# Performance work log

Hardware: AMD Instinct MI355X
Metric: run time of the kernel (lower is better)

Reference implementation:

```python
import jax, jax.numpy as jnp
import numpy as np

L = 2        # layer_depth
H = 128      # rnn_size (== embedding dim)
V = 50257    # vocab_size
B = 100      # batch_size
T = 50       # seq_length


def setup_inputs() -> dict:
    key = jax.random.key(0)
    ks = jax.random.split(key, 8)
    inp = {
        'input_data': jax.random.randint(ks[0], (B, T), 0, V, dtype=jnp.int32),
        # embedding ~ U(-0.08, 0.08) as in the original
        'embedding': jax.random.uniform(ks[1], (V, H), jnp.float32, -0.08, 0.08),
        # per-layer GRU params; input dim == H for every layer
        'gate_k': jax.random.normal(ks[2], (L, 2 * H, 2 * H), jnp.float32) * 0.05,
        'gate_b': jnp.ones((L, 2 * H), jnp.float32),  # TF GRUCell gate bias init = 1.0
        'cand_k': jax.random.normal(ks[3], (L, 2 * H, H), jnp.float32) * 0.05,
        'cand_b': jnp.zeros((L, H), jnp.float32),
        'softmax_w': jax.random.normal(ks[4], (V, H), jnp.float32) * 0.05,
        'softmax_b': jnp.zeros((V,), jnp.float32),
    }
    return inp


def _gru_scan(x_bth, gate_k, gate_b, cand_k, cand_b):
    # x_bth: [B, T, H] embedded inputs. Stacked L-layer GRU, TF GRUCell math:
    #   r,u = sigmoid([x,h] @ Wg + bg);  c = tanh([x, r*h] @ Wc + bc)
    #   h' = u*h + (1-u)*c
    x_tbh = jnp.swapaxes(x_bth, 0, 1)  # [T, B, H]
    h0 = jnp.zeros((L, x_bth.shape[0], H), x_bth.dtype)

    def step(hs, x_t):
        inp = x_t
        new_hs = []
        for l in range(L):
            h = hs[l]
            g = jax.nn.sigmoid(jnp.concatenate([inp, h], -1) @ gate_k[l] + gate_b[l])
            r, u = g[:, :H], g[:, H:]
            c = jnp.tanh(jnp.concatenate([inp, r * h], -1) @ cand_k[l] + cand_b[l])
            h_new = u * h + (1.0 - u) * c
            new_hs.append(h_new)
            inp = h_new
        return jnp.stack(new_hs), inp

    final_state, out_tbh = jax.lax.scan(step, h0, x_tbh)
    return jnp.swapaxes(out_tbh, 0, 1), final_state  # [B, T, H], [L, B, H]


def reference(input_data, embedding, gate_k, gate_b, cand_k, cand_b, softmax_w, softmax_b):
    x = embedding[input_data]                                   # [B, T, H]
    out, _ = _gru_scan(x, gate_k, gate_b, cand_k, cand_b)       # [B, T, H]
    out = out.reshape(-1, H)                                    # [B*T, H]
    logits = out @ softmax_w.T + softmax_b                      # [B*T, V]
    probs = jax.nn.softmax(logits, axis=-1)
    return logits, probs
```

## Files before the change

kernel.cpp:

```cpp
#include <hip/hip_runtime.h>
#include <hip/hip_bf16.h>
#include <math.h>

#define GL 2
#define GH 128
#define GH2 256
#define GV 50257
#define GB 100
#define GT 50
#define GM 5000
#define NT 393
#define MT 40

typedef __attribute__((ext_vector_type(4))) float f32x4;
typedef __attribute__((ext_vector_type(8))) short bf16x8;

__global__ __launch_bounds__(256) void gather_kernel(
    const int* __restrict__ tok, const float* __restrict__ emb,
    float* __restrict__ xb)
{
    const int i = blockIdx.x * 256 + threadIdx.x;
    if (i < GM * 32) {
        const int m = i >> 5, k4 = (i & 31) * 4;
        *(float4*)&xb[(size_t)m * GH + k4] =
            *(const float4*)&emb[(size_t)tok[m] * GH + k4];
    }
}

__global__ __launch_bounds__(256) void xpart_kernel(
    const float* __restrict__ in,
    const float* __restrict__ gk,
    const float* __restrict__ ck,
    float* __restrict__ gx,
    float* __restrict__ cx)
{
    __shared__ float xs[16][128];
    __shared__ float cpart[2][16][128];
    const int m0 = blockIdx.x * 16;
    const int tid = threadIdx.x;
    #pragma unroll
    for (int p = 0; p < 8; ++p) {
        const int idx = p * 256 + tid;
        const int r = idx >> 7, kq = idx & 127;
        int m = m0 + r; if (m > GM - 1) m = GM - 1;
        xs[r][kq] = in[(size_t)m * GH + kq];
    }
    __syncthreads();
    {
        float acc[16];
        #pragma unroll
        for (int r = 0; r < 16; ++r) acc[r] = 0.f;
        for (int k = 0; k < GH; ++k) {
            const float w = gk[k * GH2 + tid];
            #pragma unroll
            for (int r = 0; r < 16; ++r) acc[r] += xs[r][k] * w;
        }
        #pragma unroll
        for (int r = 0; r < 16; ++r)
            if (m0 + r < GM) gx[(size_t)(m0 + r) * GH2 + tid] = acc[r];
    }
    {
        const int j = tid & 127, kh = tid >> 7;
        float acc[16];
        #pragma unroll
        for (int r = 0; r < 16; ++r) acc[r] = 0.f;
        for (int k = kh * 64; k < kh * 64 + 64; ++k) {
            const float w = ck[k * GH + j];
            #pragma unroll
            for (int r = 0; r < 16; ++r) acc[r] += xs[r][k] * w;
        }
        #pragma unroll
        for (int r = 0; r < 16; ++r) cpart[kh][r][j] = acc[r];
    }
    __syncthreads();
    for (int idx = tid; idx < 16 * 128; idx += 256) {
        const int r = idx >> 7, j = idx & 127;
        if (m0 + r < GM) cx[(size_t)(m0 + r) * GH + j] = cpart[0][r][j] + cpart[1][r][j];
    }
}

__global__ __launch_bounds__(1024) void scan_kernel(
    const float* __restrict__ gxp,
    const float* __restrict__ cxp,
    const float* __restrict__ gkb,
    const float* __restrict__ ckb,
    const float* __restrict__ gb,
    const float* __restrict__ cb,
    float* __restrict__ hout)
{
    const int b = blockIdx.x;
    const int tid = threadIdx.x;
    const int jg = tid & 255, t4 = tid >> 8;
    const int jc = tid & 127, t8 = tid >> 7;

    float wg[32], wc[16];
    #pragma unroll
    for (int i = 0; i < 32; ++i) wg[i] = gkb[(size_t)(t4 * 32 + i) * GH2 + jg];
    #pragma unroll
    for (int i = 0; i < 16; ++i) wc[i] = ckb[(size_t)(t8 * 16 + i) * GH + jc];

    __shared__ float hs[GH];
    __shared__ float rh[GH];
    __shared__ float g[GH2];
    __shared__ float gpart[4][GH2];
    __shared__ float cpart[8][GH];
    if (tid < GH) hs[tid] = 0.f;
    __syncthreads();

    for (int t = 0; t < GT; ++t) {
        const int m = b * GT + t;
        {
            float acc = 0.f;
            #pragma unroll
            for (int i = 0; i < 32; ++i) acc += hs[t4 * 32 + i] * wg[i];
            gpart[t4][jg] = acc;
        }
        __syncthreads();
        if (tid < GH2) {
            const float s = gxp[(size_t)m * GH2 + tid] + gpart[0][tid] + gpart[1][tid]
                          + gpart[2][tid] + gpart[3][tid] + gb[tid];
            g[tid] = 1.f / (1.f + expf(-s));
        }
        __syncthreads();
        if (tid < GH) rh[tid] = g[tid] * hs[tid];
        __syncthreads();
        {
            float acc = 0.f;
            #pragma unroll
            for (int i = 0; i < 16; ++i) acc += rh[t8 * 16 + i] * wc[i];
            cpart[t8][jc] = acc;
        }
        __syncthreads();
        if (tid < GH) {
            float cs = cxp[(size_t)m * GH + tid] + cb[tid];
            #pragma unroll
            for (int p = 0; p < 8; ++p) cs += cpart[p][tid];
            const float c = tanhf(cs);
            const float u = g[GH + tid];
            const float hn = u * hs[tid] + (1.f - u) * c;
            hs[tid] = hn;
            hout[(size_t)m * GH + tid] = hn;
        }
        __syncthreads();
    }
}

__device__ __forceinline__ unsigned short f2bf(float x) {
    union { float f; unsigned u; } c; c.f = x;
    unsigned r = c.u + 0x7FFFu + ((c.u >> 16) & 1u);
    return (unsigned short)(r >> 16);
}
__device__ __forceinline__ float bf2f(unsigned short b) {
    union { unsigned u; float f; } c; c.u = ((unsigned)b) << 16; return c.f;
}

__global__ __launch_bounds__(256) void prep_kernel(
    const float* __restrict__ src, unsigned short* __restrict__ dst,
    int ntiles, int nrows)
{
    const int idx = blockIdx.x * 256 + threadIdx.x;
    if (idx >= ntiles * 4 * 128) return;
    const int r    = idx & 127;
    const int c    = idx >> 7;
    const int cs   = c & 3;
    const int tile = c >> 2;
    int row = tile * 128 + r; if (row > nrows - 1) row = nrows - 1;
    const float* s = src + (size_t)row * GH + (cs & 1) * 64;
    unsigned short* d = dst + (size_t)c * 8192 + r * 64;
    const bool lo = (cs >= 2);
    const int rx = r & 7;

    #pragma unroll
    for (int gq = 0; gq < 8; ++gq) {
        float x[8];
        *(float4*)(x)     = *(const float4*)(s + gq * 8);
        *(float4*)(x + 4) = *(const float4*)(s + gq * 8 + 4);
        unsigned u[4];
        #pragma unroll
        for (int q = 0; q < 4; ++q) {
            const float a0 = x[q * 2], a1 = x[q * 2 + 1];
            const unsigned short hi0 = f2bf(a0), hi1 = f2bf(a1);
            unsigned short h0, h1;
            if (lo) { h0 = f2bf(a0 - bf2f(hi0)); h1 = f2bf(a1 - bf2f(hi1)); }
            else    { h0 = hi0; h1 = hi1; }
            u[q] = (unsigned)h0 | ((unsigned)h1 << 16);
        }
        *(uint4*)(d + (size_t)((gq ^ rx) * 8)) = *(const uint4*)u;
    }
}

__global__ __launch_bounds__(256) void mfma_logits_kernel(
    const unsigned short* __restrict__ Ap, const unsigned short* __restrict__ Wp,
    const float* __restrict__ bias,
    float* __restrict__ logits, float* __restrict__ pmax, float* __restrict__ psum)
{
    __shared__ unsigned short ldsA[8192];
    __shared__ unsigned short ldsW[8192];
    __shared__ float sM[2][128];
    __shared__ float sS[2][128];

    const int bm  = blockIdx.x;
    const int bt  = blockIdx.y;
    const int tid = threadIdx.x;
    const int wid  = tid >> 6;
    const int lane = tid & 63;
    const int wm = wid >> 1, wn = wid & 1;
    const int l15 = lane & 15, l4 = lane >> 4;

    constexpr int amap[6] = {0, 0, 2, 1, 1, 3};
    constexpr int astg[6] = {1, 0, 1, 1, 0, 1};
    constexpr int wmap[6] = {2, 0, 0, 3, 1, 1};
    constexpr int wstg[6] = {1, 1, 0, 1, 1, 0};

    f32x4 acc[4][4];
    #pragma unroll
    for (int i = 0; i < 4; ++i)
        #pragma unroll
        for (int j = 0; j < 4; ++j) acc[i][j] = (f32x4){0.f, 0.f, 0.f, 0.f};

    #pragma unroll
    for (int s = 0; s < 6; ++s) {
        if (astg[s]) {
            const unsigned short* ga = Ap + (size_t)(bm * 4 + amap[s]) * 8192 + wid * 2048 + lane * 8;
            #pragma unroll
            for (int i = 0; i < 4; ++i)
                __builtin_amdgcn_global_load_lds(
                    (const __attribute__((address_space(1))) void*)(ga + i * 512),
                    (__attribute__((address_space(3))) void*)(&ldsA[wid * 2048 + i * 512]), 16, 0, 0);
        }
        if (wstg[s]) {
            const unsigned short* gw = Wp + (size_t)(bt * 4 + wmap[s]) * 8192 + wid * 2048 + lane * 8;
            #pragma unroll
            for (int i = 0; i < 4; ++i)
                __builtin_amdgcn_global_load_lds(
                    (const __attribute__((address_space(1))) void*)(gw + i * 512),
                    (__attribute__((address_space(3))) void*)(&ldsW[wid * 2048 + i * 512]), 16, 0, 0);
        }
        __syncthreads();

        #pragma unroll
        for (int ks = 0; ks < 2; ++ks) {
            bf16x8 af[4], bf[4];
            #pragma unroll
            for (int mi = 0; mi < 4; ++mi) {
                const int row = wm * 64 + mi * 16 + l15;
                const int off = row * 64 + ((ks * 32 + l4 * 8) ^ ((row & 7) << 3));
                af[mi] = *(const bf16x8*)&ldsA[off];
            }
            #pragma unroll
            for (int nj = 0; nj < 4; ++nj) {
                const int row = wn * 64 + nj * 16 + l15;
                const int off = row * 64 + ((ks * 32 + l4 * 8) ^ ((row & 7) << 3));
                bf[nj] = *(const bf16x8*)&ldsW[off];
            }
            #pragma unroll
            for (int mi = 0; mi < 4; ++mi)
                #pragma unroll
                for (int nj = 0; nj < 4; ++nj)
                    acc[mi][nj] = __builtin_amdgcn_mfma_f32_16x16x32_bf16(
                        bf[nj], af[mi], acc[mi][nj], 0, 0, 0);
        }
        __syncthreads();
    }

    const int n0b = bt * 128 + wn * 64;
    float bj4[4][4];
    #pragma unroll
    for (int nj = 0; nj < 4; ++nj) {
        const int nb = n0b + nj * 16 + l4 * 4;
        if (nb + 3 < GV) {
            const float4 t = *(const float4*)&bias[nb];
            bj4[nj][0] = t.x; bj4[nj][1] = t.y; bj4[nj][2] = t.z; bj4[nj][3] = t.w;
        } else {
            #pragma unroll
            for (int r = 0; r < 4; ++r) bj4[nj][r] = (nb + r < GV) ? bias[nb + r] : 0.f;
        }
    }
    #pragma unroll
    for (int mi = 0; mi < 4; ++mi) {
        const int rowb = wm * 64 + mi * 16 + l15;
        const int m = bm * 128 + rowb;
        float v[4][4];
        float mx = -INFINITY;
        #pragma unroll
        for (int nj = 0; nj < 4; ++nj)
            #pragma unroll
            for (int r = 0; r < 4; ++r) {
                v[nj][r] = acc[mi][nj][r] + bj4[nj][r];
                if (n0b + nj * 16 + l4 * 4 + r < GV) mx = fmaxf(mx, v[nj][r]);
            }
        mx = fmaxf(mx, __shfl_xor(mx, 16));
        mx = fmaxf(mx, __shfl_xor(mx, 32));
        float se = 0.f;
        #pragma unroll
        for (int nj = 0; nj < 4; ++nj)
            #pragma unroll
            for (int r = 0; r < 4; ++r)
                if (n0b + nj * 16 + l4 * 4 + r < GV) se += __expf(v[nj][r] - mx);
        se += __shfl_xor(se, 16);
        se += __shfl_xor(se, 32);
        if (m < GM) {
            float* lrow = logits + (size_t)m * GV;
            #pragma unroll
            for (int nj = 0; nj < 4; ++nj) {
                const int nb = n0b + nj * 16 + l4 * 4;
                if (nb + 3 < GV) {
                    float4 st;
                    st.x = v[nj][0]; st.y = v[nj][1]; st.z = v[nj][2]; st.w = v[nj][3];
                    *(float4*)&lrow[nb] = st;
                } else {
                    #pragma unroll
                    for (int r = 0; r < 4; ++r)
                        if (nb + r < GV) lrow[nb + r] = v[nj][r];
                }
            }
        }
        if (l4 == 0) { sM[wn][rowb] = mx; sS[wn][rowb] = se; }
    }
    __syncthreads();
    if (tid < 128) {
        const int m = bm * 128 + tid;
        if (m < GM) {
            const float m0 = sM[0][tid], m1 = sM[1][tid];
            const float M = fmaxf(m0, m1);
            const float S = sS[0][tid] * __expf(m0 - M) + sS[1][tid] * __expf(m1 - M);
            pmax[(size_t)m * NT + bt] = M;
            psum[(size_t)m * NT + bt] = S;
        }
    }
}

__global__ __launch_bounds__(64) void reduce_kernel(
    const float* __restrict__ pmax, const float* __restrict__ psum,
    float* __restrict__ rowM, float* __restrict__ rowInvS)
{
    const int m = blockIdx.x;
    const int lane = threadIdx.x;
    float M = -INFINITY, S = 0.f;
    for (int t = lane; t < NT; t += 64) {
        const float m2 = pmax[(size_t)m * NT + t];
        const float s2 = psum[(size_t)m * NT + t];
        const float nM = fmaxf(M, m2);
        S = S * expf(M - nM) + s2 * expf(m2 - nM);
        M = nM;
    }
    #pragma unroll
    for (int d = 1; d < 64; d <<= 1) {
        const float m2 = __shfl_xor(M, d);
        const float s2 = __shfl_xor(S, d);
        const float nM = fmaxf(M, m2);
        S = S * expf(M - nM) + s2 * expf(m2 - nM);
        M = nM;
    }
    if (lane == 0) { rowM[m] = M; rowInvS[m] = 1.f / S; }
}

__global__ __launch_bounds__(256) void probs_kernel(
    const float* __restrict__ logits,
    const float* __restrict__ rowM, const float* __restrict__ rowInvS,
    float* __restrict__ probs)
{
    const float4* L4 = reinterpret_cast<const float4*>(logits);
    float4* P4 = reinterpret_cast<float4*>(probs);
    const int n4 = (int)(((long long)GM * GV) / 4);
    const int stride = gridDim.x * blockDim.x;
    for (int i = blockIdx.x * blockDim.x + threadIdx.x; i < n4; i += stride) {
        const float4 v = L4[i];
        const int base = i * 4;
        const int m0 = base / GV;
        const int m3 = (base + 3) / GV;
        float4 o;
        if (m0 == m3) {
            const float M = rowM[m0], Is = rowInvS[m0];
            o.x = __expf(v.x - M) * Is;
            o.y = __expf(v.y - M) * Is;
            o.z = __expf(v.z - M) * Is;
            o.w = __expf(v.w - M) * Is;
        } else {
            const int ma = base / GV, mb = (base + 1) / GV;
            const int mc = (base + 2) / GV, md = (base + 3) / GV;
            o.x = __expf(v.x - rowM[ma]) * rowInvS[ma];
            o.y = __expf(v.y - rowM[mb]) * rowInvS[mb];
            o.z = __expf(v.z - rowM[mc]) * rowInvS[mc];
            o.w = __expf(v.w - rowM[md]) * rowInvS[md];
        }
        P4[i] = o;
    }
}

extern "C" void kernel_launch(void* const* d_in, const int* in_sizes, int n_in,
                              void* d_out, int out_size, void* d_ws, size_t ws_size,
                              hipStream_t stream) {
    const int*   tok    = (const int*)d_in[0];
    const float* emb    = (const float*)d_in[1];
    const float* gate_k = (const float*)d_in[2];
    const float* gate_b = (const float*)d_in[3];
    const float* cand_k = (const float*)d_in[4];
    const float* cand_b = (const float*)d_in[5];
    const float* W      = (const float*)d_in[6];
    const float* bias   = (const float*)d_in[7];

    float* logits = (float*)d_out;
    float* probs  = logits + (size_t)GM * GV;

    float* ws = (float*)d_ws;
    float* gruout = ws;
    unsigned short* Ap = (unsigned short*)(gruout + 640000);
    unsigned short* Wp = Ap + (size_t)MT * 4 * 8192;
    float* pmax    = (float*)(Wp + (size_t)NT * 4 * 8192);
    float* psum    = pmax + (size_t)GM * NT;
    float* rowM    = psum + (size_t)GM * NT;
    float* rowInvS = rowM + GM;

    float* XBH0 = pmax;
    float* GX   = pmax + 640000;
    float* CX   = pmax + 1920000;

    gather_kernel<<<(GM * 32 + 255) / 256, 256, 0, stream>>>(tok, emb, XBH0);
    xpart_kernel<<<(GM + 15) / 16, 256, 0, stream>>>(XBH0, gate_k, cand_k, GX, CX);
    scan_kernel<<<GB, 1024, 0, stream>>>(GX, CX,
        gate_k + 128 * GH2, cand_k + 128 * GH, gate_b, cand_b, XBH0 );
    xpart_kernel<<<(GM + 15) / 16, 256, 0, stream>>>(XBH0,
        gate_k + GH2 * GH2, cand_k + GH2 * GH, GX, CX);
    scan_kernel<<<GB, 1024, 0, stream>>>(GX, CX,
        gate_k + GH2 * GH2 + 128 * GH2, cand_k + GH2 * GH + 128 * GH,
        gate_b + GH2, cand_b + GH, gruout);

    prep_kernel<<<(MT * 4 * 128 + 255) / 256, 256, 0, stream>>>(gruout, Ap, MT, GM);
    prep_kernel<<<(NT * 4 * 128 + 255) / 256, 256, 0, stream>>>(W, Wp, NT, GV);

    dim3 g2(MT, NT);
    mfma_logits_kernel<<<g2, 256, 0, stream>>>(Ap, Wp, bias, logits, pmax, psum);

    reduce_kernel<<<GM, 64, 0, stream>>>(pmax, psum, rowM, rowInvS);

    probs_kernel<<<4096, 256, 0, stream>>>(logits, rowM, rowInvS, probs);
}
```

Baseline: 1.215 ms.

## Double-buffer LDS in logits GEMM with 32-wide K chunks

The packed bf16 layout is split into 32-column K chunks, 8 per tile covering hi/lo parts, and the logits MFMA kernel now double-buffers A and W chunks in LDS. Global-to-LDS loads for the next chunk are issued while MFMAs run on the current one, aiming to hide load latency that the earlier stage-then-sync loop exposed. LDS per block stays the same. The kernel now has more barriers and a more intricate chunk schedule that must still cover the three hi/lo product terms correctly.

Measured after the change: 1.219 ms. Within noise of the previous version (+0.3%).

```diff
diff --git a/kernel.cpp b/kernel.cpp
--- a/kernel.cpp
+++ b/kernel.cpp
@@ -159,22 +159,22 @@
     int ntiles, int nrows)
 {
     const int idx = blockIdx.x * 256 + threadIdx.x;
-    if (idx >= ntiles * 4 * 128) return;
+    if (idx >= ntiles * 8 * 128) return;
     const int r    = idx & 127;
     const int c    = idx >> 7;
-    const int cs   = c & 3;
-    const int tile = c >> 2;
+    const int cs   = c & 7;
+    const int tile = c >> 3;
     int row = tile * 128 + r; if (row > nrows - 1) row = nrows - 1;
-    const float* s = src + (size_t)row * GH + (cs & 1) * 64;
-    unsigned short* d = dst + (size_t)c * 8192 + r * 64;
-    const bool lo = (cs >= 2);
-    const int rx = r & 7;
-
-    #pragma unroll
-    for (int gq = 0; gq < 8; ++gq) {
+    const float* s = src + (size_t)row * GH + (cs & 3) * 32;
+    unsigned short* d = dst + (size_t)c * 4096 + r * 32;
+    const bool lo = (cs >= 4);
+    const int rx = r & 3;
+
+    #pragma unroll
+    for (int g = 0; g < 4; ++g) {
         float x[8];
-        *(float4*)(x)     = *(const float4*)(s + gq * 8);
-        *(float4*)(x + 4) = *(const float4*)(s + gq * 8 + 4);
+        *(float4*)(x)     = *(const float4*)(s + g * 8);
+        *(float4*)(x + 4) = *(const float4*)(s + g * 8 + 4);
         unsigned u[4];
         #pragma unroll
         for (int q = 0; q < 4; ++q) {
@@ -185,7 +185,7 @@
             else    { h0 = hi0; h1 = hi1; }
             u[q] = (unsigned)h0 | ((unsigned)h1 << 16);
         }
-        *(uint4*)(d + (size_t)((gq ^ rx) * 8)) = *(const uint4*)u;
+        *(uint4*)(d + (size_t)((g ^ rx) * 8)) = *(const uint4*)u;
     }
 }
 
@@ -194,74 +194,78 @@
     const float* __restrict__ bias,
     float* __restrict__ logits, float* __restrict__ pmax, float* __restrict__ psum)
 {
-    __shared__ unsigned short ldsA[8192];
-    __shared__ unsigned short ldsW[8192];
+    __shared__ unsigned short ldsA[2][4096];
+    __shared__ unsigned short ldsW[2][4096];
     __shared__ float sM[2][128];
     __shared__ float sS[2][128];
 
     const int bm  = blockIdx.x;
     const int bt  = blockIdx.y;
     const int tid = threadIdx.x;
+    const int lane = tid & 63;
     const int wid  = tid >> 6;
-    const int lane = tid & 63;
     const int wm = wid >> 1, wn = wid & 1;
     const int l15 = lane & 15, l4 = lane >> 4;
 
-    constexpr int amap[6] = {0, 0, 2, 1, 1, 3};
-    constexpr int astg[6] = {1, 0, 1, 1, 0, 1};
-    constexpr int wmap[6] = {2, 0, 0, 3, 1, 1};
-    constexpr int wstg[6] = {1, 1, 0, 1, 1, 0};
-
     f32x4 acc[4][4];
     #pragma unroll
     for (int i = 0; i < 4; ++i)
         #pragma unroll
         for (int j = 0; j < 4; ++j) acc[i][j] = (f32x4){0.f, 0.f, 0.f, 0.f};
 
-    #pragma unroll
-    for (int s = 0; s < 6; ++s) {
-        if (astg[s]) {
-            const unsigned short* ga = Ap + (size_t)(bm * 4 + amap[s]) * 8192 + wid * 2048 + lane * 8;
-            #pragma unroll
-            for (int i = 0; i < 4; ++i)
-                __builtin_amdgcn_global_load_lds(
-                    (const __attribute__((address_space(1))) void*)(ga + i * 512),
-                    (__attribute__((address_space(3))) void*)(&ldsA[wid * 2048 + i * 512]), 16, 0, 0);
-        }
-        if (wstg[s]) {
-            const unsigned short* gw = Wp + (size_t)(bt * 4 + wmap[s]) * 8192 + wid * 2048 + lane * 8;
-            #pragma unroll
-            for (int i = 0; i < 4; ++i)
-                __builtin_amdgcn_global_load_lds(
-                    (const __attribute__((address_space(1))) void*)(gw + i * 512),
-                    (__attribute__((address_space(3))) void*)(&ldsW[wid * 2048 + i * 512]), 16, 0, 0);
-        }
-        __syncthreads();
-
-        #pragma unroll
-        for (int ks = 0; ks < 2; ++ks) {
-            bf16x8 af[4], bf[4];
-            #pragma unroll
-            for (int mi = 0; mi < 4; ++mi) {
-                const int row = wm * 64 + mi * 16 + l15;
-                const int off = row * 64 + ((ks * 32 + l4 * 8) ^ ((row & 7) << 3));
-                af[mi] = *(const bf16x8*)&ldsA[off];
-            }
-            #pragma unroll
-            for (int nj = 0; nj < 4; ++nj) {
-                const int row = wn * 64 + nj * 16 + l15;
-                const int off = row * 64 + ((ks * 32 + l4 * 8) ^ ((row & 7) << 3));
-                bf[nj] = *(const bf16x8*)&ldsW[off];
-            }
-            #pragma unroll
-            for (int mi = 0; mi < 4; ++mi)
-                #pragma unroll
-                for (int nj = 0; nj < 4; ++nj)
-                    acc[mi][nj] = __builtin_amdgcn_mfma_f32_16x16x32_bf16(
-                        bf[nj], af[mi], acc[mi][nj], 0, 0, 0);
-        }
-        __syncthreads();
-    }
+#define STAGE(SLOT, PTR, TILE, CH)                                                      \
+    {                                                                                   \
+        const unsigned short* g_ = (PTR) + (size_t)(TILE) * 32768 + (CH) * 4096 + tid * 8; \
+        __builtin_amdgcn_global_load_lds(                                               \
+            (const __attribute__((address_space(1))) void*)(g_),                        \
+            (__attribute__((address_space(3))) void*)(&(SLOT)[tid * 8]), 16, 0, 0);     \
+        __builtin_amdgcn_global_load_lds(                                               \
+            (const __attribute__((address_space(1))) void*)(g_ + 2048),                 \
+            (__attribute__((address_space(3))) void*)(&(SLOT)[tid * 8 + 2048]), 16, 0, 0); \
+    }
+#define COMPUTE(ASL, WSL)                                                               \
+    {                                                                                   \
+        bf16x8 af[4], bf[4];                                                            \
+        _Pragma("unroll")                                                               \
+        for (int mi = 0; mi < 4; ++mi) {                                                \
+            const int row = wm * 64 + mi * 16 + l15;                                    \
+            const int off = row * 32 + ((l4 * 8) ^ ((row & 3) << 3));                   \
+            af[mi] = *(const bf16x8*)&(ASL)[off];                                       \
+        }                                                                               \
+        _Pragma("unroll")                                                               \
+        for (int nj = 0; nj < 4; ++nj) {                                                \
+            const int row = wn * 64 + nj * 16 + l15;                                    \
+            const int off = row * 32 + ((l4 * 8) ^ ((row & 3) << 3));                   \
+            bf[nj] = *(const bf16x8*)&(WSL)[off];                                       \
+        }                                                                               \
+        _Pragma("unroll")                                                               \
+        for (int mi = 0; mi < 4; ++mi)                                                  \
+            _Pragma("unroll")                                                           \
+            for (int nj = 0; nj < 4; ++nj)                                              \
+                acc[mi][nj] = __builtin_amdgcn_mfma_f32_16x16x32_bf16(                  \
+                    bf[nj], af[mi], acc[mi][nj], 0, 0, 0);                              \
+    }
+
+    STAGE(ldsA[0], Ap, bm, 0); STAGE(ldsW[0], Wp, bt, 4);
+    __syncthreads();
+
+    #pragma unroll
+    for (int i = 0; i < 4; ++i) {
+        STAGE(ldsW[1], Wp, bt, i);
+        COMPUTE(ldsA[0], ldsW[0]);
+        __syncthreads();
+        STAGE(ldsA[1], Ap, bm, 4 + i);
+        COMPUTE(ldsA[0], ldsW[1]);
+        __syncthreads();
+        if (i < 3) {
+            STAGE(ldsA[0], Ap, bm, i + 1);
+            STAGE(ldsW[0], Wp, bt, 4 + i + 1);
+        }
+        COMPUTE(ldsA[1], ldsW[1]);
+        __syncthreads();
+    }
+#undef STAGE
+#undef COMPUTE
 
     const int n0b = bt * 128 + wn * 64;
     float bj4[4][4];
@@ -406,8 +410,8 @@
     float* ws = (float*)d_ws;
     float* gruout = ws;
     unsigned short* Ap = (unsigned short*)(gruout + 640000);
-    unsigned short* Wp = Ap + (size_t)MT * 4 * 8192;
-    float* pmax    = (float*)(Wp + (size_t)NT * 4 * 8192);
+    unsigned short* Wp = Ap + (size_t)MT * 32768;
+    float* pmax    = (float*)(Wp + (size_t)NT * 32768);
     float* psum    = pmax + (size_t)GM * NT;
     float* rowM    = psum + (size_t)GM * NT;
     float* rowInvS = rowM + GM;
@@ -426,8 +430,8 @@
         gate_k + GH2 * GH2 + 128 * GH2, cand_k + GH2 * GH + 128 * GH,
         gate_b + GH2, cand_b + GH, gruout);
 
-    prep_kernel<<<(MT * 4 * 128 + 255) / 256, 256, 0, stream>>>(gruout, Ap, MT, GM);
-    prep_kernel<<<(NT * 4 * 128 + 255) / 256, 256, 0, stream>>>(W, Wp, NT, GV);
+    prep_kernel<<<(MT * 8 * 128 + 255) / 256, 256, 0, stream>>>(gruout, Ap, MT, GM);
+    prep_kernel<<<(NT * 8 * 128 + 255) / 256, 256, 0, stream>>>(W, Wp, NT, GV);
 
     dim3 g2(MT, NT);
     mfma_logits_kernel<<<g2, 256, 0, stream>>>(Ap, Wp, bias, logits, pmax, psum);
```

## Overlap softmax weight bf16 prep with first-layer GRU scan in one launch

Applied to the files above, without the earlier changes.

Merges the softmax-weight split-bf16 conversion into the layer-0 scan kernel by appending extra blocks that run prep work while the 100 scan blocks execute the serial recurrence. The intent is to hide the weight-prep kernel's time behind the latency-bound scan, which leaves most CUs idle, and to remove one launch. The risk is that prep blocks, at 1024 threads, compete with scan blocks for CUs and memory bandwidth, or inherit the scan kernel's register and LDS footprint.

New measurement: 1.209 ms. About the same (-0.5%).

```diff
diff --git a/kernel.cpp b/kernel.cpp
--- a/kernel.cpp
+++ b/kernel.cpp
@@ -15,136 +15,6 @@
 typedef __attribute__((ext_vector_type(4))) float f32x4;
 typedef __attribute__((ext_vector_type(8))) short bf16x8;
 
-__global__ __launch_bounds__(256) void gather_kernel(
-    const int* __restrict__ tok, const float* __restrict__ emb,
-    float* __restrict__ xb)
-{
-    const int i = blockIdx.x * 256 + threadIdx.x;
-    if (i < GM * 32) {
-        const int m = i >> 5, k4 = (i & 31) * 4;
-        *(float4*)&xb[(size_t)m * GH + k4] =
-            *(const float4*)&emb[(size_t)tok[m] * GH + k4];
-    }
-}
-
-__global__ __launch_bounds__(256) void xpart_kernel(
-    const float* __restrict__ in,
-    const float* __restrict__ gk,
-    const float* __restrict__ ck,
-    float* __restrict__ gx,
-    float* __restrict__ cx)
-{
-    __shared__ float xs[16][128];
-    __shared__ float cpart[2][16][128];
-    const int m0 = blockIdx.x * 16;
-    const int tid = threadIdx.x;
-    #pragma unroll
-    for (int p = 0; p < 8; ++p) {
-        const int idx = p * 256 + tid;
-        const int r = idx >> 7, kq = idx & 127;
-        int m = m0 + r; if (m > GM - 1) m = GM - 1;
-        xs[r][kq] = in[(size_t)m * GH + kq];
-    }
-    __syncthreads();
-    {
-        float acc[16];
-        #pragma unroll
-        for (int r = 0; r < 16; ++r) acc[r] = 0.f;
-        for (int k = 0; k < GH; ++k) {
-            const float w = gk[k * GH2 + tid];
-            #pragma unroll
-            for (int r = 0; r < 16; ++r) acc[r] += xs[r][k] * w;
-        }
-        #pragma unroll
-        for (int r = 0; r < 16; ++r)
-            if (m0 + r < GM) gx[(size_t)(m0 + r) * GH2 + tid] = acc[r];
-    }
-    {
-        const int j = tid & 127, kh = tid >> 7;
-        float acc[16];
-        #pragma unroll
-        for (int r = 0; r < 16; ++r) acc[r] = 0.f;
-        for (int k = kh * 64; k < kh * 64 + 64; ++k) {
-            const float w = ck[k * GH + j];
-            #pragma unroll
-            for (int r = 0; r < 16; ++r) acc[r] += xs[r][k] * w;
-        }
-        #pragma unroll
-        for (int r = 0; r < 16; ++r) cpart[kh][r][j] = acc[r];
-    }
-    __syncthreads();
-    for (int idx = tid; idx < 16 * 128; idx += 256) {
-        const int r = idx >> 7, j = idx & 127;
-        if (m0 + r < GM) cx[(size_t)(m0 + r) * GH + j] = cpart[0][r][j] + cpart[1][r][j];
-    }
-}
-
-__global__ __launch_bounds__(1024) void scan_kernel(
-    const float* __restrict__ gxp,
-    const float* __restrict__ cxp,
-    const float* __restrict__ gkb,
-    const float* __restrict__ ckb,
-    const float* __restrict__ gb,
-    const float* __restrict__ cb,
-    float* __restrict__ hout)
-{
-    const int b = blockIdx.x;
-    const int tid = threadIdx.x;
-    const int jg = tid & 255, t4 = tid >> 8;
-    const int jc = tid & 127, t8 = tid >> 7;
-
-    float wg[32], wc[16];
-    #pragma unroll
-    for (int i = 0; i < 32; ++i) wg[i] = gkb[(size_t)(t4 * 32 + i) * GH2 + jg];
-    #pragma unroll
-    for (int i = 0; i < 16; ++i) wc[i] = ckb[(size_t)(t8 * 16 + i) * GH + jc];
-
-    __shared__ float hs[GH];
-    __shared__ float rh[GH];
-    __shared__ float g[GH2];
-    __shared__ float gpart[4][GH2];
-    __shared__ float cpart[8][GH];
-    if (tid < GH) hs[tid] = 0.f;
-    __syncthreads();
-
-    for (int t = 0; t < GT; ++t) {
-        const int m = b * GT + t;
-        {
-            float acc = 0.f;
-            #pragma unroll
-            for (int i = 0; i < 32; ++i) acc += hs[t4 * 32 + i] * wg[i];
-            gpart[t4][jg] = acc;
-        }
-        __syncthreads();
-        if (tid < GH2) {
-            const float s = gxp[(size_t)m * GH2 + tid] + gpart[0][tid] + gpart[1][tid]
-                          + gpart[2][tid] + gpart[3][tid] + gb[tid];
-            g[tid] = 1.f / (1.f + expf(-s));
-        }
-        __syncthreads();
-        if (tid < GH) rh[tid] = g[tid] * hs[tid];
-        __syncthreads();
-        {
-            float acc = 0.f;
-            #pragma unroll
-            for (int i = 0; i < 16; ++i) acc += rh[t8 * 16 + i] * wc[i];
-            cpart[t8][jc] = acc;
-        }
-        __syncthreads();
-        if (tid < GH) {
-            float cs = cxp[(size_t)m * GH + tid] + cb[tid];
-            #pragma unroll
-            for (int p = 0; p < 8; ++p) cs += cpart[p][tid];
-            const float c = tanhf(cs);
-            const float u = g[GH + tid];
-            const float hn = u * hs[tid] + (1.f - u) * c;
-            hs[tid] = hn;
-            hout[(size_t)m * GH + tid] = hn;
-        }
-        __syncthreads();
-    }
-}
-
 __device__ __forceinline__ unsigned short f2bf(float x) {
     union { float f; unsigned u; } c; c.f = x;
     unsigned r = c.u + 0x7FFFu + ((c.u >> 16) & 1u);
@@ -154,12 +24,10 @@
     union { unsigned u; float f; } c; c.u = ((unsigned)b) << 16; return c.f;
 }
 
-__global__ __launch_bounds__(256) void prep_kernel(
+__device__ __forceinline__ void prep_one(
     const float* __restrict__ src, unsigned short* __restrict__ dst,
-    int ntiles, int nrows)
-{
-    const int idx = blockIdx.x * 256 + threadIdx.x;
-    if (idx >= ntiles * 4 * 128) return;
+    int idx, int nrows)
+{
     const int r    = idx & 127;
     const int c    = idx >> 7;
     const int cs   = c & 3;
@@ -187,6 +55,165 @@
         }
         *(uint4*)(d + (size_t)((gq ^ rx) * 8)) = *(const uint4*)u;
     }
+}
+
+__global__ __launch_bounds__(256) void gather_kernel(
+    const int* __restrict__ tok, const float* __restrict__ emb,
+    float* __restrict__ xb)
+{
+    const int i = blockIdx.x * 256 + threadIdx.x;
+    if (i < GM * 32) {
+        const int m = i >> 5, k4 = (i & 31) * 4;
+        *(float4*)&xb[(size_t)m * GH + k4] =
+            *(const float4*)&emb[(size_t)tok[m] * GH + k4];
+    }
+}
+
+__global__ __launch_bounds__(256) void xpart_kernel(
+    const float* __restrict__ in,
+    const float* __restrict__ gk,
+    const float* __restrict__ ck,
+    float* __restrict__ gx,
+    float* __restrict__ cx)
+{
+    __shared__ float xs[16][128];
+    __shared__ float cpart[2][16][128];
+    const int m0 = blockIdx.x * 16;
+    const int tid = threadIdx.x;
+    #pragma unroll
+    for (int p = 0; p < 8; ++p) {
+        const int idx = p * 256 + tid;
+        const int r = idx >> 7, kq = idx & 127;
+        int m = m0 + r; if (m > GM - 1) m = GM - 1;
+        xs[r][kq] = in[(size_t)m * GH + kq];
+    }
+    __syncthreads();
+    {
+        float acc[16];
+        #pragma unroll
+        for (int r = 0; r < 16; ++r) acc[r] = 0.f;
+        for (int k = 0; k < GH; ++k) {
+            const float w = gk[k * GH2 + tid];
+            #pragma unroll
+            for (int r = 0; r < 16; ++r) acc[r] += xs[r][k] * w;
+        }
+        #pragma unroll
+        for (int r = 0; r < 16; ++r)
+            if (m0 + r < GM) gx[(size_t)(m0 + r) * GH2 + tid] = acc[r];
+    }
+    {
+        const int j = tid & 127, kh = tid >> 7;
+        float acc[16];
+        #pragma unroll
+        for (int r = 0; r < 16; ++r) acc[r] = 0.f;
+        for (int k = kh * 64; k < kh * 64 + 64; ++k) {
+            const float w = ck[k * GH + j];
+            #pragma unroll
+            for (int r = 0; r < 16; ++r) acc[r] += xs[r][k] * w;
+        }
+        #pragma unroll
+        for (int r = 0; r < 16; ++r) cpart[kh][r][j] = acc[r];
+    }
+    __syncthreads();
+    for (int idx = tid; idx < 16 * 128; idx += 256) {
+        const int r = idx >> 7, j = idx & 127;
+        if (m0 + r < GM) cx[(size_t)(m0 + r) * GH + j] = cpart[0][r][j] + cpart[1][r][j];
+    }
+}
+
+__device__ __forceinline__ void scan_body(
+    int b, int tid,
+    const float* __restrict__ gxp, const float* __restrict__ cxp,
+    const float* __restrict__ gkb, const float* __restrict__ ckb,
+    const float* __restrict__ gb,  const float* __restrict__ cb,
+    float* __restrict__ hout)
+{
+    const int jg = tid & 255, t4 = tid >> 8;
+    const int jc = tid & 127, t8 = tid >> 7;
+
+    float wg[32], wc[16];
+    #pragma unroll
+    for (int i = 0; i < 32; ++i) wg[i] = gkb[(size_t)(t4 * 32 + i) * GH2 + jg];
+    #pragma unroll
+    for (int i = 0; i < 16; ++i) wc[i] = ckb[(size_t)(t8 * 16 + i) * GH + jc];
+
+    __shared__ float hs[GH];
+    __shared__ float rh[GH];
+    __shared__ float g[GH2];
+    __shared__ float gpart[4][GH2];
+    __shared__ float cpart[8][GH];
+    if (tid < GH) hs[tid] = 0.f;
+    __syncthreads();
+
+    for (int t = 0; t < GT; ++t) {
+        const int m = b * GT + t;
+        {
+            float acc = 0.f;
+            #pragma unroll
+            for (int i = 0; i < 32; ++i) acc += hs[t4 * 32 + i] * wg[i];
+            gpart[t4][jg] = acc;
+        }
+        __syncthreads();
+        if (tid < GH2) {
+            const float s = gxp[(size_t)m * GH2 + tid] + gpart[0][tid] + gpart[1][tid]
+                          + gpart[2][tid] + gpart[3][tid] + gb[tid];
+            g[tid] = 1.f / (1.f + expf(-s));
+        }
+        __syncthreads();
+        if (tid < GH) rh[tid] = g[tid] * hs[tid];
+        __syncthreads();
+        {
+            float acc = 0.f;
+            #pragma unroll
+            for (int i = 0; i < 16; ++i) acc += rh[t8 * 16 + i] * wc[i];
+            cpart[t8][jc] = acc;
+        }
+        __syncthreads();
+        if (tid < GH) {
+            float cs = cxp[(size_t)m * GH + tid] + cb[tid];
+            #pragma unroll
+            for (int p = 0; p < 8; ++p) cs += cpart[p][tid];
+            const float c = tanhf(cs);
+            const float u = g[GH + tid];
+            const float hn = u * hs[tid] + (1.f - u) * c;
+            hs[tid] = hn;
+            hout[(size_t)m * GH + tid] = hn;
+        }
+        __syncthreads();
+    }
+}
+
+__global__ __launch_bounds__(1024) void scan_kernel(
+    const float* __restrict__ gxp, const float* __restrict__ cxp,
+    const float* __restrict__ gkb, const float* __restrict__ ckb,
+    const float* __restrict__ gb,  const float* __restrict__ cb,
+    float* __restrict__ hout)
+{
+    scan_body(blockIdx.x, threadIdx.x, gxp, cxp, gkb, ckb, gb, cb, hout);
+}
+
+__global__ __launch_bounds__(1024) void scan_prepw_kernel(
+    const float* __restrict__ gxp, const float* __restrict__ cxp,
+    const float* __restrict__ gkb, const float* __restrict__ ckb,
+    const float* __restrict__ gb,  const float* __restrict__ cb,
+    float* __restrict__ hout,
+    const float* __restrict__ W, unsigned short* __restrict__ Wp)
+{
+    if (blockIdx.x < GB) {
+        scan_body(blockIdx.x, threadIdx.x, gxp, cxp, gkb, ckb, gb, cb, hout);
+    } else {
+        const int idx = (blockIdx.x - GB) * 1024 + threadIdx.x;
+        if (idx < NT * 4 * 128) prep_one(W, Wp, idx, GV);
+    }
+}
+
+__global__ __launch_bounds__(256) void prep_kernel(
+    const float* __restrict__ src, unsigned short* __restrict__ dst,
+    int ntiles, int nrows)
+{
+    const int idx = blockIdx.x * 256 + threadIdx.x;
+    if (idx >= ntiles * 4 * 128) return;
+    prep_one(src, dst, idx, nrows);
 }
 
 __global__ __launch_bounds__(256) void mfma_logits_kernel(
@@ -418,8 +445,10 @@
 
     gather_kernel<<<(GM * 32 + 255) / 256, 256, 0, stream>>>(tok, emb, XBH0);
     xpart_kernel<<<(GM + 15) / 16, 256, 0, stream>>>(XBH0, gate_k, cand_k, GX, CX);
-    scan_kernel<<<GB, 1024, 0, stream>>>(GX, CX,
-        gate_k + 128 * GH2, cand_k + 128 * GH, gate_b, cand_b, XBH0 );
+    const int prepw_blocks = (NT * 4 * 128 + 1023) / 1024;
+    scan_prepw_kernel<<<GB + prepw_blocks, 1024, 0, stream>>>(GX, CX,
+        gate_k + 128 * GH2, cand_k + 128 * GH, gate_b, cand_b, XBH0 ,
+        W, Wp);
     xpart_kernel<<<(GM + 15) / 16, 256, 0, stream>>>(XBH0,
         gate_k + GH2 * GH2, cand_k + GH2 * GH, GX, CX);
     scan_kernel<<<GB, 1024, 0, stream>>>(GX, CX,
@@ -427,7 +456,6 @@
         gate_b + GH2, cand_b + GH, gruout);
 
     prep_kernel<<<(MT * 4 * 128 + 255) / 256, 256, 0, stream>>>(gruout, Ap, MT, GM);
-    prep_kernel<<<(NT * 4 * 128 + 255) / 256, 256, 0, stream>>>(W, Wp, NT, GV);
 
     dim3 g2(MT, NT);
     mfma_logits_kernel<<<g2, 256, 0, stream>>>(Ap, Wp, bias, logits, pmax, psum);
```
